# Kernel tuning notes

Measured on AMD Instinct MI355X. Metric: run time of the kernel, lower is better.

The kernel has to match this reference:

```python
import jax, jax.numpy as jnp
import numpy as np

EPS = 1e-12  # undefined global `eps` in the original source; standard tiny epsilon


def setup_inputs() -> dict:
    key = jax.random.key(0)
    k1, k2 = jax.random.split(key)
    B, C = 32768, 1000
    output = jax.random.normal(k1, (B, C), dtype=jnp.float32)
    multilabels = (jax.random.uniform(k2, (B, C)) < 0.05).astype(jnp.float32)
    multilabels = multilabels.at[:, 0].set(1.0)
    return {"output": output, "multilabels": multilabels}


def reference(output, multilabels):
    # Equivalent closed form of: for every nonempty subset g of true labels,
    #   loss(g) = -[ pseudo_y*log(o+eps) + (1-pseudo_y)*log(1-o+eps) ].sum()
    #           = base - sum_{j in g} gain_j,
    # with base = -sum_j log(1-o_j+eps) and gain_j = log(o_j+eps)-log(1-o_j+eps).
    # min over nonempty subsets = base - max nonempty-subset gain
    #   = base - (sum of positive gains over true labels, or the max single
    #      gain among true labels if all gains are negative).
    o = jax.nn.sigmoid(output)                      # [B, C]
    log_p = jnp.log(o + EPS)
    log_np = jnp.log(1.0 - o + EPS)
    base = -jnp.sum(log_np, axis=1)                 # [B]
    gain = log_p - log_np                           # [B, C]
    is_true = multilabels == 1.0                    # [B, C] bool (constant)
    pos = is_true & (gain > 0)
    pos_gain = jnp.sum(jnp.where(pos, gain, 0.0), axis=1)          # [B]
    any_pos = jnp.any(pos, axis=1)                                  # [B]
    best_single = jnp.max(jnp.where(is_true, gain, -jnp.inf), axis=1)  # [B]
    max_gain = jnp.where(any_pos, pos_gain, best_single)
    per_sample = base - max_gain                    # [B]
    return jnp.mean(per_sample)
```

## Files before the change

### kernel.cpp

```cpp
#include <hip/hip_runtime.h>
#include <math.h>


constexpr int B = 32768;
constexpr int C = 1000;
constexpr int C4 = C / 4;
constexpr int THREADS = 256;

typedef float f32x4 __attribute__((ext_vector_type(4)));

__device__ __forceinline__ void elem_update(float x, float m,
                                            float& base, float& pos, float& best) {
    float e  = __expf(-fabsf(x));
    float xp = fmaxf(x, 0.0f);
    base += xp + __logf(1.0f + e);
    pos  += m * xp;
    if (m != 0.0f) best = fmaxf(best, x);
}

__global__ __launch_bounds__(THREADS)
void row_loss_kernel(const float* __restrict__ X,
                     const float* __restrict__ M,
                     float* __restrict__ partial) {
    const int row = blockIdx.x;
    const int t   = threadIdx.x;

    float base = 0.f, pos = 0.f, best = -INFINITY;

    if (t < C4) {
        const f32x4* x4 = reinterpret_cast<const f32x4*>(X + (size_t)row * C);
        const f32x4* m4 = reinterpret_cast<const f32x4*>(M + (size_t)row * C);
        f32x4 x = __builtin_nontemporal_load(x4 + t);
        f32x4 m = __builtin_nontemporal_load(m4 + t);
        elem_update(x.x, m.x, base, pos, best);
        elem_update(x.y, m.y, base, pos, best);
        elem_update(x.z, m.z, base, pos, best);
        elem_update(x.w, m.w, base, pos, best);
    }

    #pragma unroll
    for (int off = 32; off > 0; off >>= 1) {
        base += __shfl_down(base, off, 64);
        pos  += __shfl_down(pos,  off, 64);
        best  = fmaxf(best, __shfl_down(best, off, 64));
    }

    __shared__ float sb[4], sp[4], ss[4];
    const int w    = t >> 6;
    const int lane = t & 63;
    if (lane == 0) { sb[w] = base; sp[w] = pos; ss[w] = best; }
    __syncthreads();
    if (t == 0) {
        float b = (sb[0] + sb[1]) + (sb[2] + sb[3]);
        float p = (sp[0] + sp[1]) + (sp[2] + sp[3]);
        float s = fmaxf(fmaxf(ss[0], ss[1]), fmaxf(ss[2], ss[3]));
        partial[row] = b - ((p > 0.f) ? p : s);
    }
}

__global__ __launch_bounds__(256)
void finalize1_kernel(const float* __restrict__ partial, float* __restrict__ mid) {
    const int b = blockIdx.x;
    const int t = threadIdx.x;
    float v = partial[b * 512 + t] + partial[b * 512 + t + 256];

    #pragma unroll
    for (int off = 32; off > 0; off >>= 1)
        v += __shfl_down(v, off, 64);

    __shared__ float s[4];
    const int w    = t >> 6;
    const int lane = t & 63;
    if (lane == 0) s[w] = v;
    __syncthreads();
    if (t == 0) mid[b] = (s[0] + s[1]) + (s[2] + s[3]);
}

__global__ __launch_bounds__(64)
void finalize2_kernel(const float* __restrict__ mid, float* __restrict__ out) {
    double v = (double)mid[threadIdx.x];
    #pragma unroll
    for (int off = 32; off > 0; off >>= 1)
        v += __shfl_down(v, off, 64);
    if (threadIdx.x == 0) out[0] = (float)(v / (double)B);
}

extern "C" void kernel_launch(void* const* d_in, const int* in_sizes, int n_in,
                              void* d_out, int out_size, void* d_ws, size_t ws_size,
                              hipStream_t stream) {
    const float* X  = (const float*)d_in[0];
    const float* M  = (const float*)d_in[1];
    float* out      = (float*)d_out;
    float* partial  = (float*)d_ws;
    float* mid      = partial + B;

    row_loss_kernel<<<B, THREADS, 0, stream>>>(X, M, partial);
    finalize1_kernel<<<64, 256, 0, stream>>>(partial, mid);
    finalize2_kernel<<<1, 64, 0, stream>>>(mid, out);
}
```

Baseline: 246.1 us.

## Process eight rows per wave with double-buffered register prefetch

Each row is now handled by a single 64-lane wave instead of a 256-thread block, and each wave walks eight consecutive rows. The next row's loads are issued into a second register buffer before the current row is computed. This removes the LDS and __syncthreads cross-wave reduction, launches far fewer blocks, and overlaps memory latency with compute. In exchange it uses more registers per thread, and with only 1024 blocks there may be fewer waves in flight to hide latency on a bandwidth-bound kernel.

```diff
diff --git a/kernel.cpp b/kernel.cpp
--- a/kernel.cpp
+++ b/kernel.cpp
@@ -6,6 +6,9 @@
 constexpr int C = 1000;
 constexpr int C4 = C / 4;
 constexpr int THREADS = 256;
+constexpr int WAVES_PER_BLOCK = THREADS / 64;
+constexpr int ROWS_PER_WAVE = 8;
+constexpr int NBLOCKS = B / (WAVES_PER_BLOCK * ROWS_PER_WAVE);
 
 typedef float f32x4 __attribute__((ext_vector_type(4)));
 
@@ -18,43 +21,69 @@
     if (m != 0.0f) best = fmaxf(best, x);
 }
 
-__global__ __launch_bounds__(THREADS)
-void row_loss_kernel(const float* __restrict__ X,
-                     const float* __restrict__ M,
-                     float* __restrict__ partial) {
-    const int row = blockIdx.x;
-    const int t   = threadIdx.x;
+__device__ __forceinline__ void load_row(const float* __restrict__ Xrow,
+                                         const float* __restrict__ Mrow,
+                                         int lane,
+                                         f32x4 (&xb)[4], f32x4 (&mb)[4]) {
+    const f32x4* x4 = reinterpret_cast<const f32x4*>(Xrow);
+    const f32x4* m4 = reinterpret_cast<const f32x4*>(Mrow);
+    #pragma unroll
+    for (int j = 0; j < 4; ++j) {
+        const int idx = j * 64 + lane;
+        if (idx < C4) {
+            xb[j] = __builtin_nontemporal_load(x4 + idx);
+            mb[j] = __builtin_nontemporal_load(m4 + idx);
+        }
+    }
+}
 
+__device__ __forceinline__ float row_result(int lane,
+                                            const f32x4 (&xb)[4],
+                                            const f32x4 (&mb)[4]) {
     float base = 0.f, pos = 0.f, best = -INFINITY;
-
-    if (t < C4) {
-        const f32x4* x4 = reinterpret_cast<const f32x4*>(X + (size_t)row * C);
-        const f32x4* m4 = reinterpret_cast<const f32x4*>(M + (size_t)row * C);
-        f32x4 x = __builtin_nontemporal_load(x4 + t);
-        f32x4 m = __builtin_nontemporal_load(m4 + t);
-        elem_update(x.x, m.x, base, pos, best);
-        elem_update(x.y, m.y, base, pos, best);
-        elem_update(x.z, m.z, base, pos, best);
-        elem_update(x.w, m.w, base, pos, best);
+    #pragma unroll
+    for (int j = 0; j < 4; ++j) {
+        const int idx = j * 64 + lane;
+        if (idx < C4) {
+            elem_update(xb[j].x, mb[j].x, base, pos, best);
+            elem_update(xb[j].y, mb[j].y, base, pos, best);
+            elem_update(xb[j].z, mb[j].z, base, pos, best);
+            elem_update(xb[j].w, mb[j].w, base, pos, best);
+        }
     }
-
     #pragma unroll
     for (int off = 32; off > 0; off >>= 1) {
         base += __shfl_down(base, off, 64);
         pos  += __shfl_down(pos,  off, 64);
         best  = fmaxf(best, __shfl_down(best, off, 64));
     }
+    return base - ((pos > 0.f) ? pos : best);
+}
 
-    __shared__ float sb[4], sp[4], ss[4];
-    const int w    = t >> 6;
-    const int lane = t & 63;
-    if (lane == 0) { sb[w] = base; sp[w] = pos; ss[w] = best; }
-    __syncthreads();
-    if (t == 0) {
-        float b = (sb[0] + sb[1]) + (sb[2] + sb[3]);
-        float p = (sp[0] + sp[1]) + (sp[2] + sp[3]);
-        float s = fmaxf(fmaxf(ss[0], ss[1]), fmaxf(ss[2], ss[3]));
-        partial[row] = b - ((p > 0.f) ? p : s);
+__global__ __launch_bounds__(THREADS)
+void row_loss_kernel(const float* __restrict__ X,
+                     const float* __restrict__ M,
+                     float* __restrict__ partial) {
+    const int wid  = blockIdx.x * WAVES_PER_BLOCK + (threadIdx.x >> 6);
+    const int lane = threadIdx.x & 63;
+    const int row0 = wid * ROWS_PER_WAVE;
+
+    f32x4 xa[4], ma[4], xc[4], mc[4];
+
+    load_row(X + (size_t)row0 * C, M + (size_t)row0 * C, lane, xa, ma);
+
+    #pragma unroll
+    for (int k = 0; k < ROWS_PER_WAVE; ++k) {
+        const int r = row0 + k;
+        if (k + 1 < ROWS_PER_WAVE) {
+            const float* Xn = X + (size_t)(r + 1) * C;
+            const float* Mn = M + (size_t)(r + 1) * C;
+            if (k & 1) load_row(Xn, Mn, lane, xa, ma);
+            else       load_row(Xn, Mn, lane, xc, mc);
+        }
+        const float res = (k & 1) ? row_result(lane, xc, mc)
+                                  : row_result(lane, xa, ma);
+        if (lane == 0) partial[r] = res;
     }
 }
 
@@ -94,7 +123,7 @@
     float* partial  = (float*)d_ws;
     float* mid      = partial + B;
 
-    row_loss_kernel<<<B, THREADS, 0, stream>>>(X, M, partial);
+    row_loss_kernel<<<NBLOCKS, THREADS, 0, stream>>>(X, M, partial);
     finalize1_kernel<<<64, 256, 0, stream>>>(partial, mid);
     finalize2_kernel<<<1, 64, 0, stream>>>(mid, out);
 }
```

After: 251.2 us. 2.1% more time.

## Process rows per wave with direct global-to-LDS loads in a persistent grid

Applied to the files above, without the earlier changes.

The row kernel changes from one 256-thread block per row to one 64-lane wave per row, with a fixed grid of 2048 blocks. Each wave loops over 4 strided rows. Rows are staged into LDS with 16-byte global_load_lds instructions, then each lane reads 4 float4 vectors and the row is reduced with wave shuffles only, so the shared-memory cross-wave step and __syncthreads go away. The aim is to cut per-block launch and synchronisation overhead and use lanes better, at the cost of 32KB of LDS per block. That LDS use limits occupancy, and each wave waits on vmcnt(0) for every row with no prefetch of the next one, which may reduce memory-level parallelism.

```diff
diff --git a/kernel.cpp b/kernel.cpp
--- a/kernel.cpp
+++ b/kernel.cpp
@@ -1,13 +1,20 @@
 #include <hip/hip_runtime.h>
 #include <math.h>
+#include <stdint.h>
 
 
 constexpr int B = 32768;
 constexpr int C = 1000;
 constexpr int C4 = C / 4;
 constexpr int THREADS = 256;
+constexpr int WAVES_PER_BLOCK = THREADS / 64;
+constexpr int NBLOCKS = 2048;
+constexpr int TOTAL_WAVES = NBLOCKS * WAVES_PER_BLOCK;
+constexpr int ROWS_PER_WAVE = B / TOTAL_WAVES;
 
 typedef float f32x4 __attribute__((ext_vector_type(4)));
+typedef __attribute__((address_space(3))) void lds_void_t;
+typedef const __attribute__((address_space(1))) void gbl_void_t;
 
 __device__ __forceinline__ void elem_update(float x, float m,
                                             float& base, float& pos, float& best) {
@@ -18,43 +25,56 @@
     if (m != 0.0f) best = fmaxf(best, x);
 }
 
+__device__ __forceinline__ void gld_lds16(const void* gsrc, void* ldst) {
+    __builtin_amdgcn_global_load_lds((gbl_void_t*)gsrc, (lds_void_t*)ldst,
+                                     16, 0, 0);
+}
+
 __global__ __launch_bounds__(THREADS)
 void row_loss_kernel(const float* __restrict__ X,
                      const float* __restrict__ M,
                      float* __restrict__ partial) {
-    const int row = blockIdx.x;
-    const int t   = threadIdx.x;
+    __shared__ __align__(16) float ldsX[WAVES_PER_BLOCK][1024];
+    __shared__ __align__(16) float ldsM[WAVES_PER_BLOCK][1024];
 
-    float base = 0.f, pos = 0.f, best = -INFINITY;
+    const int w    = threadIdx.x >> 6;
+    const int lane = threadIdx.x & 63;
+    const int wid  = blockIdx.x * WAVES_PER_BLOCK + w;
 
-    if (t < C4) {
-        const f32x4* x4 = reinterpret_cast<const f32x4*>(X + (size_t)row * C);
-        const f32x4* m4 = reinterpret_cast<const f32x4*>(M + (size_t)row * C);
-        f32x4 x = __builtin_nontemporal_load(x4 + t);
-        f32x4 m = __builtin_nontemporal_load(m4 + t);
-        elem_update(x.x, m.x, base, pos, best);
-        elem_update(x.y, m.y, base, pos, best);
-        elem_update(x.z, m.z, base, pos, best);
-        elem_update(x.w, m.w, base, pos, best);
-    }
+    for (int k = 0; k < ROWS_PER_WAVE; ++k) {
+        const int r = wid + k * TOTAL_WAVES;
+        const f32x4* x4 = reinterpret_cast<const f32x4*>(X + (size_t)r * C);
+        const f32x4* m4 = reinterpret_cast<const f32x4*>(M + (size_t)r * C);
 
-    #pragma unroll
-    for (int off = 32; off > 0; off >>= 1) {
-        base += __shfl_down(base, off, 64);
-        pos  += __shfl_down(pos,  off, 64);
-        best  = fmaxf(best, __shfl_down(best, off, 64));
-    }
+        #pragma unroll
+        for (int j = 0; j < 4; ++j) {
+            const int idx = min(j * 64 + lane, C4 - 1);
+            gld_lds16((const void*)(x4 + idx), (void*)&ldsX[w][j * 256]);
+            gld_lds16((const void*)(m4 + idx), (void*)&ldsM[w][j * 256]);
+        }
+        asm volatile("s_waitcnt vmcnt(0)" ::: "memory");
+        __builtin_amdgcn_sched_barrier(0);
 
-    __shared__ float sb[4], sp[4], ss[4];
-    const int w    = t >> 6;
-    const int lane = t & 63;
-    if (lane == 0) { sb[w] = base; sp[w] = pos; ss[w] = best; }
-    __syncthreads();
-    if (t == 0) {
-        float b = (sb[0] + sb[1]) + (sb[2] + sb[3]);
-        float p = (sp[0] + sp[1]) + (sp[2] + sp[3]);
-        float s = fmaxf(fmaxf(ss[0], ss[1]), fmaxf(ss[2], ss[3]));
-        partial[row] = b - ((p > 0.f) ? p : s);
+        float base = 0.f, pos = 0.f, best = -INFINITY;
+        #pragma unroll
+        for (int j = 0; j < 4; ++j) {
+            const int idx = j * 64 + lane;
+            if (idx < C4) {
+                f32x4 x = *reinterpret_cast<const f32x4*>(&ldsX[w][j * 256 + lane * 4]);
+                f32x4 m = *reinterpret_cast<const f32x4*>(&ldsM[w][j * 256 + lane * 4]);
+                elem_update(x.x, m.x, base, pos, best);
+                elem_update(x.y, m.y, base, pos, best);
+                elem_update(x.z, m.z, base, pos, best);
+                elem_update(x.w, m.w, base, pos, best);
+            }
+        }
+        #pragma unroll
+        for (int off = 32; off > 0; off >>= 1) {
+            base += __shfl_down(base, off, 64);
+            pos  += __shfl_down(pos,  off, 64);
+            best  = fmaxf(best, __shfl_down(best, off, 64));
+        }
+        if (lane == 0) partial[r] = base - ((pos > 0.f) ? pos : best);
     }
 }
 
@@ -94,7 +114,7 @@
     float* partial  = (float*)d_ws;
     float* mid      = partial + B;
 
-    row_loss_kernel<<<B, THREADS, 0, stream>>>(X, M, partial);
+    row_loss_kernel<<<NBLOCKS, THREADS, 0, stream>>>(X, M, partial);
     finalize1_kernel<<<64, 256, 0, stream>>>(partial, mid);
     finalize2_kernel<<<1, 64, 0, stream>>>(mid, out);
 }
```

New measurement: 276.7 us. 12.4% more time.
